# Kernel tuning notes

Measured on AMD Instinct MI355X. Metric: run time of the kernel, lower is better.

Reference implementation:

```python
import jax, jax.numpy as jnp
import numpy as np

D, D_SEQ, D_HEAD, N_HEAD = 256, 1280, 48, 8
N_NODE, B_GRAPH, S_LEN = 2048, 8, 1024
HDH = N_HEAD * D_HEAD  # 384
SCALE = float(np.sqrt(D_HEAD))
LN_EPS = 1e-5


def setup_inputs() -> dict:
    key = jax.random.key(0)
    ks = jax.random.split(key, 12)
    node = jax.random.normal(ks[0], (N_NODE, D), dtype=jnp.float32)
    emb = jax.random.normal(ks[1], (B_GRAPH, S_LEN, D_SEQ), dtype=jnp.float32)
    mask = jax.random.randint(ks[2], (B_GRAPH, S_LEN), 0, 2, dtype=jnp.int32)
    batch = jnp.sort(jax.random.randint(ks[3], (N_NODE,), 0, B_GRAPH, dtype=jnp.int64))
    def lin(k, fan_in, fan_out):
        lim = 1.0 / np.sqrt(fan_in)
        return jax.random.uniform(k, (fan_in, fan_out), jnp.float32, -lim, lim)
    return {
        "node": node,
        "packed_sequence_emb": emb,
        "packed_sequence_mask": mask,
        "batch": batch,
        "ln_g": jnp.ones((D,), jnp.float32),
        "ln_b": jnp.zeros((D,), jnp.float32),
        "Wq": lin(ks[4], D, HDH),
        "Wk": lin(ks[5], D_SEQ, HDH),
        "Wv": lin(ks[6], D_SEQ, HDH),
        "Wg": lin(ks[7], D, HDH),
        "bg": jnp.zeros((HDH,), jnp.float32),
        "Wback": lin(ks[8], HDH, D),
        "bback": jnp.zeros((D,), jnp.float32),
    }


def _layernorm(x, g, b):
    mu = jnp.mean(x, axis=-1, keepdims=True)
    var = jnp.mean(jnp.square(x - mu), axis=-1, keepdims=True)
    return (x - mu) * jax.lax.rsqrt(var + LN_EPS) * g + b


def reference(node, packed_sequence_emb, packed_sequence_mask, batch,
              ln_g, ln_b, Wq, Wk, Wv, Wg, bg, Wback, bback):
    N = node.shape[0]
    y = _layernorm(node, ln_g, ln_b)                                   # [N, D]
    q = (y @ Wq).reshape(N, N_HEAD, D_HEAD)                            # [N, H, Dh]
    k = (packed_sequence_emb @ Wk).reshape(B_GRAPH, S_LEN, N_HEAD, D_HEAD)
    v = (packed_sequence_emb @ Wv).reshape(B_GRAPH, S_LEN, N_HEAD, D_HEAD)

    # scores[n, s, h] = <q[n,h], k[batch[n], s, h]> / sqrt(Dh)
    scores_all = jnp.einsum('nhd,bshd->nbsh', q, k) / SCALE            # [N, B, S, H]
    scores = jnp.take_along_axis(
        scores_all, batch[:, None, None, None].astype(jnp.int32), axis=1
    )[:, 0]                                                            # [N, S, H]

    # masked softmax over sequence axis (dim=1), mask broadcast over heads
    mask_f = packed_sequence_mask[batch].astype(scores.dtype)[:, :, None]  # [N, S, 1]
    s_max = jnp.max(jnp.where(mask_f > 0, scores, -jnp.inf), axis=1, keepdims=True)
    e = jnp.exp(scores - s_max) * mask_f
    w = e / (jnp.sum(e, axis=1, keepdims=True) + 1e-9)                 # [N, S, H]

    # out[n,h,d] = sum_s w[n,s,h] * v[batch[n], s, h, d]
    feat_all = jnp.einsum('nsh,bshd->nbhd', w, v)                      # [N, B, H, Dh]
    feat = jnp.take_along_axis(
        feat_all, batch[:, None, None, None].astype(jnp.int32), axis=1
    )[:, 0]                                                            # [N, H, Dh]

    gate = jax.nn.sigmoid(y @ Wg + bg).reshape(N, N_HEAD, D_HEAD)
    new = (gate * feat).reshape(N, HDH) @ Wback + bback
    return node + new
```

## Files before the change

### kernel.cpp

```cpp
#include <hip/hip_runtime.h>
#include <hip/hip_bf16.h>
#include <math.h>

#define D 256
#define D_SEQ 1280
#define D_HEAD 48
#define N_HEAD 8
#define HDH 384
#define N_NODE 2048
#define B_GRAPH 8
#define S_LEN 1024
#define LN_EPS 1e-5f
#define QSCALE (0.14433756729740643f * 1.4426950408889634f)
#define KVN 768
#define QGN 768
#define QROWS (N_NODE + 16)
#define TPG 40
#define NWL (TPG * 8)
#define PAD_T 164864

typedef unsigned short u16;
typedef __attribute__((ext_vector_type(8))) short short8;
typedef __attribute__((ext_vector_type(4))) short short4v;
typedef __attribute__((ext_vector_type(4))) unsigned short ushort4v;
typedef __attribute__((ext_vector_type(4))) float floatx4;

__device__ __forceinline__ u16 f2bf(float f) {
    unsigned int x = __float_as_uint(f);
    x += 0x7fff + ((x >> 16) & 1);
    return (u16)(x >> 16);
}

__device__ __forceinline__ void load_lds16(const u16* g, u16* lds) {
    __builtin_amdgcn_global_load_lds(
        (const __attribute__((address_space(1))) unsigned int*)g,
        (__attribute__((address_space(3))) unsigned int*)lds, 16, 0, 0);
}

__global__ __launch_bounds__(256)
void prep(const float* __restrict__ emb, u16* __restrict__ embb,
          const float* __restrict__ node, const float* __restrict__ ln_g,
          const float* __restrict__ ln_b, u16* __restrict__ yb,
          const float* __restrict__ Wk, const float* __restrict__ Wv,
          const float* __restrict__ Wq, const float* __restrict__ Wg,
          const float* __restrict__ Wback,
          u16* __restrict__ WT, u16* __restrict__ WT2, u16* __restrict__ WbT,
          const int* __restrict__ batch, const int* __restrict__ mask,
          int* __restrict__ ranges, int* __restrict__ wl,
          int* __restrict__ kvwl, int* __restrict__ scnt,
          u16* __restrict__ Kp, u16* __restrict__ Qb) {
    const int bx = blockIdx.x;
    const int tid = threadIdx.x;
    if (bx < 512) {
        const int b = bx >> 6, chunk = bx & 63;
        __shared__ unsigned long long words[16];
        __shared__ int wpre[17];
        #pragma unroll
        for (int c = 0; c < 4; ++c) {
            const int s = c * 256 + tid;
            const unsigned long long bal = __ballot(mask[b * S_LEN + s] != 0);
            if ((tid & 63) == 0) words[c * 4 + (tid >> 6)] = bal;
        }
        __syncthreads();
        if (tid == 0) {
            int a = 0;
            #pragma unroll
            for (int w = 0; w < 16; ++w) { wpre[w] = a; a += __popcll(words[w]); }
            wpre[16] = a;
        }
        __syncthreads();
        const int cnt = wpre[16];
        const int ce = (cnt + 127) & ~127;
        const int r = chunk * 16 + (tid >> 4);
        const int sub = tid & 15;
        const unsigned long long w = words[r >> 6];
        const bool on = (w >> (r & 63)) & 1ull;
        if (on) {
            const int rank = wpre[r >> 6] +
                __popcll(w & ((1ull << (r & 63)) - 1ull));
            const float* src = &emb[((size_t)b * S_LEN + r) * D_SEQ];
            u16* dst = &embb[((size_t)b * S_LEN + rank) * D_SEQ];
            #pragma unroll
            for (int it = 0; it < 10; ++it) {
                const int off = it * 128 + sub * 8;
                const float4 a = *(const float4*)&src[off];
                const float4 b4 = *(const float4*)&src[off + 4];
                union { u16 u[8]; int4 v; } p;
                p.u[0]=f2bf(a.x); p.u[1]=f2bf(a.y); p.u[2]=f2bf(a.z); p.u[3]=f2bf(a.w);
                p.u[4]=f2bf(b4.x); p.u[5]=f2bf(b4.y); p.u[6]=f2bf(b4.z); p.u[7]=f2bf(b4.w);
                *(int4*)&dst[off] = p.v;
            }
        }
        const int c2 = chunk * 16 + (tid >> 4);
        if (c2 >= cnt && c2 < ce) {
            u16* dst = &embb[((size_t)b * S_LEN + c2) * D_SEQ];
            const int4 z = {0, 0, 0, 0};
            #pragma unroll
            for (int it = 0; it < 10; ++it)
                *(int4*)&dst[it * 128 + sub * 8] = z;
        }
        return;
    }
    if (bx < 2560) {
        const int n = bx - 512, t = tid;
        float x = node[n * D + t];
        float s = x, sq = x * x;
        #pragma unroll
        for (int o = 32; o > 0; o >>= 1) {
            s  += __shfl_down(s, o);
            sq += __shfl_down(sq, o);
        }
        __shared__ float ss[4], sqs[4];
        if ((t & 63) == 0) { ss[t >> 6] = s; sqs[t >> 6] = sq; }
        __syncthreads();
        float S  = ss[0] + ss[1] + ss[2] + ss[3];
        float SQ = sqs[0] + sqs[1] + sqs[2] + sqs[3];
        float mu  = S * (1.f / D);
        float var = SQ * (1.f / D) - mu * mu;
        float inv = rsqrtf(var + LN_EPS);
        yb[n * D + t] = f2bf((x - mu) * inv * ln_g[t] + ln_b[t]);
        return;
    }
    if (bx < 3808) {
        int u = bx - 2560;
        const float* W; u16* WTo; int K, kx, ny, Ncols;
        if (u < 480)      { W = Wk;    WTo = WT;                       K = D_SEQ; Ncols = HDH; kx = u % 40; ny = u / 40; }
        else if (u < 960) { u -= 480;  W = Wv; WTo = WT + (size_t)HDH * D_SEQ; K = D_SEQ; Ncols = HDH; kx = u % 40; ny = u / 40; }
        else if (u < 1056){ u -= 960;  W = Wq; WTo = WT2;              K = D;   Ncols = HDH; kx = u % 8;  ny = u / 8; }
        else if (u < 1152){ u -= 1056; W = Wg; WTo = WT2 + (size_t)HDH * D; K = D; Ncols = HDH; kx = u % 8; ny = u / 8; }
        else              { u -= 1152; W = Wback; WTo = WbT;           K = HDH; Ncols = D;   kx = u % 12; ny = u / 12; }
        const int k0 = kx * 32, n0 = ny * 32;
        __shared__ float tile[32][33];
        const int tx = tid & 31, ty = tid >> 5;
        #pragma unroll
        for (int i = 0; i < 32; i += 8)
            tile[ty + i][tx] = W[(size_t)(k0 + ty + i) * Ncols + n0 + tx];
        __syncthreads();
        #pragma unroll
        for (int i = 0; i < 32; i += 8)
            WTo[(size_t)(n0 + ty + i) * K + k0 + tx] = f2bf(tile[tx][ty + i]);
        return;
    }
    if (bx == 3808) {
        const int t = tid;
        __shared__ int msum[8][32];
        __shared__ int mcnt[8];
        const int g = t >> 5, ii = t & 31;
        int p = 0;
        #pragma unroll
        for (int k = 0; k < 32; ++k) p += mask[g * S_LEN + k * 32 + ii];
        msum[g][ii] = p;
        if (t <= B_GRAPH) {
            int lo = 0, hi = N_NODE;
            while (lo < hi) {
                int mid = (lo + hi) >> 1;
                if (batch[mid] < t) lo = mid + 1; else hi = mid;
            }
            ranges[t] = lo;
        }
        __syncthreads();
        if (t < 8) {
            int s = 0;
            #pragma unroll
            for (int k = 0; k < 32; ++k) s += msum[t][k];
            mcnt[t] = s;
            scnt[t] = s;
        }
        __syncthreads();
        if (t < B_GRAPH) {
            const int s = ranges[t];
            const int ntile = (ranges[t + 1] - s + 15) >> 4;
            for (int i = 0; i < TPG; ++i)
                wl[i * 8 + t] = (i < ntile) ? ((t << 16) | (s + i * 16)) : -1;
            const int tc = (mcnt[t] + 127) >> 7;
            for (int i = 0; i < 8; ++i)
                kvwl[i * 8 + t] = (i < tc) ? (t * S_LEN + i * 128) : -1;
        }
        return;
    }
    const int t = (bx - 3809) * 256 + tid;
    const int4 z = {0, 0, 0, 0};
    if (t < 131072) {
        const int row = t >> 1, half = t & 1;
        *(int4*)&Kp[(size_t)row * 64 + 48 + half * 8] = z;
    } else if (t < 164096) {
        const int u = t - 131072;
        const int row = u >> 1, half = u & 1;
        *(int4*)&Qb[(size_t)row * 64 + 48 + half * 8] = z;
    } else {
        const int u = t - 164096;
        const int row = u / 6, c = u - row * 6;
        const int hh = row >> 4, m = 2048 + (row & 15);
        *(int4*)&Qb[((size_t)hh * QROWS + m) * 64 + c * 8] = z;
    }
}

__global__ __launch_bounds__(256)
void kvqg_gemm(const u16* __restrict__ A, const u16* __restrict__ WT,
               u16* __restrict__ Kp, u16* __restrict__ V4,
               const u16* __restrict__ Ab, const u16* __restrict__ WT2,
               const float* __restrict__ bg, u16* __restrict__ Qb,
               float* __restrict__ gate, const int* __restrict__ kvwl) {
    __shared__ __align__(16) u16 As[128 * 32];
    __shared__ __align__(16) u16 Bs[64 * 32];
    const int tid = threadIdx.x;
    const int lane = tid & 63, wave = tid >> 6;
    const int wm64 = (wave >> 1) * 64, wn32 = (wave & 1) * 32;
    const int lm = lane & 15, lq = lane >> 4;

    if (blockIdx.x < 768) {
        const int e = kvwl[blockIdx.x / 12];
        if (e < 0) return;
        const int m0 = e;
        const int n0 = (blockIdx.x % 12) * 64;

        floatx4 acc[4][2] = {};

        const int srow = lane >> 2, scol = (lane & 3) * 8;
        const u16* ag  = &A[(size_t)(m0 + wave * 16 + srow) * D_SEQ + scol];
        const u16* ag2 = ag + (size_t)64 * D_SEQ;
        const u16* bgp = &WT[(size_t)(n0 + wave * 16 + srow) * D_SEQ + scol];
        u16* asb  = &As[wave * 512];
        u16* asb2 = &As[2048 + wave * 512];
        u16* bsb  = &Bs[wave * 512];

        for (int k0 = 0; k0 < D_SEQ; k0 += 32) {
            __syncthreads();
            load_lds16(ag + k0, asb);
            load_lds16(ag2 + k0, asb2);
            load_lds16(bgp + k0, bsb);
            __syncthreads();

            short8 af[4], bfr[2];
            #pragma unroll
            for (int i = 0; i < 4; ++i)
                af[i] = *(const short8*)&As[(wm64 + i * 16 + lm) * 32 + lq * 8];
            #pragma unroll
            for (int j = 0; j < 2; ++j)
                bfr[j] = *(const short8*)&Bs[(wn32 + j * 16 + lm) * 32 + lq * 8];
            #pragma unroll
            for (int i = 0; i < 4; ++i)
                #pragma unroll
                for (int j = 0; j < 2; ++j)
                    acc[i][j] = __builtin_amdgcn_mfma_f32_16x16x32_bf16(
                        af[i], bfr[j], acc[i][j], 0, 0, 0);
        }

        #pragma unroll
        for (int i = 0; i < 4; ++i) {
            const int mrow = m0 + wm64 + i * 16 + lq * 4;
            const int bb = mrow >> 10, s = mrow & 1023;
            #pragma unroll
            for (int j = 0; j < 2; ++j) {
                const int n = n0 + wn32 + j * 16 + lm;
                if (n < HDH) {
                    const int hh = n / 48, dd = n - hh * 48;
                    u16* kp = &Kp[(((size_t)(bb * N_HEAD + hh)) * S_LEN + s) * 64 + dd];
                    kp[0]   = f2bf(acc[i][j][0]);
                    kp[64]  = f2bf(acc[i][j][1]);
                    kp[128] = f2bf(acc[i][j][2]);
                    kp[192] = f2bf(acc[i][j][3]);
                } else {
                    const int nv = n - HDH;
                    const int hh = nv / 48, dd = nv - hh * 48;
                    ushort4v pk;
                    pk[0] = f2bf(acc[i][j][0]); pk[1] = f2bf(acc[i][j][1]);
                    pk[2] = f2bf(acc[i][j][2]); pk[3] = f2bf(acc[i][j][3]);
                    *(ushort4v*)&V4[(((size_t)(bb * N_HEAD + hh)) * (S_LEN / 4) + (s >> 2)) * 192 + dd * 4] = pk;
                }
            }
        }
        return;
    }

    {
        const int u = blockIdx.x - 768;
        const int m0 = (u / 12) * 128, n0 = (u % 12) * 64;

        floatx4 acc[4][2] = {};
        const int sr = tid >> 2;
        const int sc = (tid & 3) * 8;

        for (int k0 = 0; k0 < D; k0 += 32) {
            const int4 a0 = *(const int4*)&Ab[(size_t)(m0 + sr) * D + k0 + sc];
            const int4 a1 = *(const int4*)&Ab[(size_t)(m0 + sr + 64) * D + k0 + sc];
            const int4 b0 = *(const int4*)&WT2[(size_t)(n0 + sr) * D + k0 + sc];
            __syncthreads();
            *(int4*)&As[sr * 32 + sc] = a0;
            *(int4*)&As[(sr + 64) * 32 + sc] = a1;
            *(int4*)&Bs[sr * 32 + sc] = b0;
            __syncthreads();

            short8 af[4], bfr[2];
            #pragma unroll
            for (int i = 0; i < 4; ++i)
                af[i] = *(const short8*)&As[(wm64 + i * 16 + lm) * 32 + lq * 8];
            #pragma unroll
            for (int j = 0; j < 2; ++j)
                bfr[j] = *(const short8*)&Bs[(wn32 + j * 16 + lm) * 32 + lq * 8];
            #pragma unroll
            for (int i = 0; i < 4; ++i)
                #pragma unroll
                for (int j = 0; j < 2; ++j)
                    acc[i][j] = __builtin_amdgcn_mfma_f32_16x16x32_bf16(
                        af[i], bfr[j], acc[i][j], 0, 0, 0);
        }

        #pragma unroll
        for (int i = 0; i < 4; ++i) {
            const int mb = m0 + wm64 + i * 16 + lq * 4;
            #pragma unroll
            for (int j = 0; j < 2; ++j) {
                const int n = n0 + wn32 + j * 16 + lm;
                #pragma unroll
                for (int r = 0; r < 4; ++r) {
                    const int m = mb + r;
                    const float v = acc[i][j][r];
                    if (n < HDH) {
                        const int hh = n / 48, dd = n - hh * 48;
                        Qb[((size_t)hh * QROWS + m) * 64 + dd] = f2bf(v * QSCALE);
                    } else {
                        const int ng = n - HDH;
                        gate[(size_t)m * HDH + ng] = 1.f / (1.f + __expf(-(v + bg[ng])));
                    }
                }
            }
        }
    }
}

__global__ __launch_bounds__(256)
void back_gemm(const u16* __restrict__ Ab, const u16* __restrict__ Bt,
               const float* __restrict__ bias, const float* __restrict__ resid,
               float* __restrict__ C) {
    __shared__ __align__(16) u16 As[128 * 32];
    __shared__ __align__(16) u16 Bs[64 * 32];
    const int tid = threadIdx.x;
    const int lane = tid & 63, wave = tid >> 6;
    const int wm = (wave >> 1) * 64, wn = (wave & 1) * 32;
    const int m0 = blockIdx.y * 128, n0 = blockIdx.x * 64;
    const int lm = lane & 15, lq = lane >> 4;

    floatx4 acc[4][2] = {};
    const int sr = tid >> 2;
    const int sc = (tid & 3) * 8;

    for (int k0 = 0; k0 < HDH; k0 += 32) {
        const int4 a0 = *(const int4*)&Ab[(size_t)(m0 + sr) * HDH + k0 + sc];
        const int4 a1 = *(const int4*)&Ab[(size_t)(m0 + sr + 64) * HDH + k0 + sc];
        const int4 b0 = *(const int4*)&Bt[(size_t)(n0 + sr) * HDH + k0 + sc];
        __syncthreads();
        *(int4*)&As[sr * 32 + sc] = a0;
        *(int4*)&As[(sr + 64) * 32 + sc] = a1;
        *(int4*)&Bs[sr * 32 + sc] = b0;
        __syncthreads();

        short8 af[4], bfr[2];
        #pragma unroll
        for (int i = 0; i < 4; ++i)
            af[i] = *(const short8*)&As[(wm + i * 16 + lm) * 32 + lq * 8];
        #pragma unroll
        for (int j = 0; j < 2; ++j)
            bfr[j] = *(const short8*)&Bs[(wn + j * 16 + lm) * 32 + lq * 8];
        #pragma unroll
        for (int i = 0; i < 4; ++i)
            #pragma unroll
            for (int j = 0; j < 2; ++j)
                acc[i][j] = __builtin_amdgcn_mfma_f32_16x16x32_bf16(
                    af[i], bfr[j], acc[i][j], 0, 0, 0);
    }

    #pragma unroll
    for (int i = 0; i < 4; ++i) {
        const int mb = m0 + wm + i * 16 + lq * 4;
        #pragma unroll
        for (int j = 0; j < 2; ++j) {
            const int n = n0 + wn + j * 16 + lm;
            #pragma unroll
            for (int r = 0; r < 4; ++r) {
                const int m = mb + r;
                C[(size_t)m * D + n] = acc[i][j][r] + bias[n] + resid[(size_t)m * D + n];
            }
        }
    }
}

struct Pref {
    short8 k0, k1;
    short4v v0, v1, v2;
};

__device__ __forceinline__ Pref ldpref(const u16* kbase, const u16* vbase,
                                       int s, int lm, int lq) {
    Pref p;
    const u16* kr = &kbase[(size_t)(s + lm) * 64];
    p.k0 = *(const short8*)&kr[lq * 8];
    p.k1 = *(const short8*)&kr[32 + lq * 8];
    const size_t vo = (size_t)((s >> 2) + lq) * 192;
    p.v0 = *(const short4v*)&vbase[vo];
    p.v1 = *(const short4v*)&vbase[vo + 64];
    p.v2 = *(const short4v*)&vbase[vo + 128];
    return p;
}

__global__ __launch_bounds__(256)
void attn_mfma(const u16* __restrict__ Qb, const u16* __restrict__ Kp,
               const u16* __restrict__ V4, const int* __restrict__ scnt,
               const int* __restrict__ ranges, const int* __restrict__ wl,
               const float* __restrict__ gate, u16* __restrict__ gfeatb) {
    const int e = wl[blockIdx.x];
    if (e < 0) return;
    const int b = e >> 16, n0 = e & 0xffff;
    const int h = blockIdx.y;
    const int nend = ranges[b + 1];
    const int NT = min(16, nend - n0);

    const int tid = threadIdx.x;
    const int wave = tid >> 6, lane = tid & 63;
    const int lm = lane & 15, lq = lane >> 4;
    const int bh = b * N_HEAD + h;

    const u16* qrow = &Qb[((size_t)h * QROWS + n0 + lm) * 64];
    const short8 qf0 = *(const short8*)&qrow[lq * 8];
    const short8 qf1 = *(const short8*)&qrow[32 + lq * 8];

    const u16* kbase = &Kp[(size_t)bh * S_LEN * 64];
    const u16* vbase = &V4[(size_t)bh * (S_LEN / 4) * 192 + (size_t)lm * 4];

    const int cnt = scnt[b];
    const int T = (cnt + 15) >> 4;
    const int j = wave;
    const int nt = (j < T) ? (((T - 1 - j) >> 2) + 1) : 0;

    float l_i = 0.f;
    floatx4 acc0 = {}, acc1 = {}, acc2 = {};

    Pref pA, pB;
    if (nt > 0) pA = ldpref(kbase, vbase, j * 16, lm, lq);
    if (nt > 1) pB = ldpref(kbase, vbase, (j + 4) * 16, lm, lq);

    int t = 0;
    auto step = [&](Pref& P) {
        const int s0 = (j + t * 4) * 16;
        floatx4 st = {};
        st = __builtin_amdgcn_mfma_f32_16x16x32_bf16(P.k0, qf0, st, 0, 0, 0);
        st = __builtin_amdgcn_mfma_f32_16x16x32_bf16(P.k1, qf1, st, 0, 0, 0);
        const short4v v0 = P.v0, v1 = P.v1, v2 = P.v2;
        if (t + 2 < nt) P = ldpref(kbase, vbase, (j + (t + 2) * 4) * 16, lm, lq);

        const int rem = cnt - s0 - lq * 4;
        const float p0 = rem > 0 ? exp2f(st[0]) : 0.f;
        const float p1 = rem > 1 ? exp2f(st[1]) : 0.f;
        const float p2 = rem > 2 ? exp2f(st[2]) : 0.f;
        const float p3 = rem > 3 ? exp2f(st[3]) : 0.f;
        l_i += (p0 + p1) + (p2 + p3);

        union { __hip_bfloat162 h2[2]; short4v v; } pu;
        pu.h2[0] = __float22bfloat162_rn(make_float2(p0, p1));
        pu.h2[1] = __float22bfloat162_rn(make_float2(p2, p3));

        acc0 = __builtin_amdgcn_mfma_f32_16x16x16bf16_1k(v0, pu.v, acc0, 0, 0, 0);
        acc1 = __builtin_amdgcn_mfma_f32_16x16x16bf16_1k(v1, pu.v, acc1, 0, 0, 0);
        acc2 = __builtin_amdgcn_mfma_f32_16x16x16bf16_1k(v2, pu.v, acc2, 0, 0, 0);
        ++t;
    };
    while (t < nt) {
        step(pA);
        if (t < nt) step(pB);
    }

    l_i += __shfl_xor(l_i, 16);
    l_i += __shfl_xor(l_i, 32);

    __shared__ float sl[4][64];
    __shared__ float sacc[4][3][4][64];
    sl[wave][lane] = l_i;
    #pragma unroll
    for (int r = 0; r < 4; ++r) {
        sacc[wave][0][r][lane] = acc0[r];
        sacc[wave][1][r][lane] = acc1[r];
        sacc[wave][2][r][lane] = acc2[r];
    }
    __syncthreads();
    if (wave < 3 && lm < NT) {
        const int dt = wave;
        const float L = sl[0][lane] + sl[1][lane] + sl[2][lane] + sl[3][lane];
        const float inv = 1.f / (L + 1e-9f);
        const size_t o = (size_t)(n0 + lm) * HDH + h * 48 + dt * 16 + lq * 4;
        const float4 g = *(const float4*)&gate[o];
        float4 ov;
        ov.x = sacc[0][dt][0][lane] + sacc[1][dt][0][lane] +
               sacc[2][dt][0][lane] + sacc[3][dt][0][lane];
        ov.y = sacc[0][dt][1][lane] + sacc[1][dt][1][lane] +
               sacc[2][dt][1][lane] + sacc[3][dt][1][lane];
        ov.z = sacc[0][dt][2][lane] + sacc[1][dt][2][lane] +
               sacc[2][dt][2][lane] + sacc[3][dt][2][lane];
        ov.w = sacc[0][dt][3][lane] + sacc[1][dt][3][lane] +
               sacc[2][dt][3][lane] + sacc[3][dt][3][lane];
        union { __hip_bfloat162 h2[2]; ushort4v v; } r2;
        r2.h2[0] = __float22bfloat162_rn(make_float2(ov.x * inv * g.x,
                                                     ov.y * inv * g.y));
        r2.h2[1] = __float22bfloat162_rn(make_float2(ov.z * inv * g.z,
                                                     ov.w * inv * g.w));
        *(ushort4v*)&gfeatb[o] = r2.v;
    }
}

extern "C" void kernel_launch(void* const* d_in, const int* in_sizes, int n_in,
                              void* d_out, int out_size, void* d_ws, size_t ws_size,
                              hipStream_t stream) {
    const float* node  = (const float*)d_in[0];
    const float* emb   = (const float*)d_in[1];
    const int*   mask  = (const int*)d_in[2];
    const int*   batch = (const int*)d_in[3];
    const float* ln_g  = (const float*)d_in[4];
    const float* ln_b  = (const float*)d_in[5];
    const float* Wq    = (const float*)d_in[6];
    const float* Wk    = (const float*)d_in[7];
    const float* Wv    = (const float*)d_in[8];
    const float* Wg    = (const float*)d_in[9];
    const float* bg    = (const float*)d_in[10];
    const float* Wback = (const float*)d_in[11];
    const float* bback = (const float*)d_in[12];
    float* out = (float*)d_out;

    float* ws    = (float*)d_ws;
    float* gate  = ws;
    float* Pacc  = gate + (size_t)N_NODE * HDH;
    float* Pl    = Pacc + (size_t)2 * N_NODE * HDH;
    u16*   gfeatb = (u16*)(Pl + (size_t)2 * N_NODE * N_HEAD);
    u16*   yb    = gfeatb + (size_t)N_NODE * HDH;
    u16*   WT    = yb + (size_t)N_NODE * D;
    u16*   WT2   = WT + (size_t)KVN * D_SEQ;
    u16*   WbT   = WT2 + (size_t)QGN * D;
    u16*   Qb    = WbT + (size_t)D * HDH;
    u16*   Kp    = Qb + (size_t)N_HEAD * QROWS * 64;
    u16*   V4    = Kp + (size_t)B_GRAPH * N_HEAD * S_LEN * 64;
    u16*   embb  = V4 + (size_t)B_GRAPH * N_HEAD * (S_LEN / 4) * 192;
    int*   ranges = (int*)(embb + (size_t)B_GRAPH * S_LEN * D_SEQ);
    int*   wl    = ranges + 16;
    int*   kvwl  = wl + NWL;
    int*   scnt  = kvwl + 64;

    prep<<<3809 + PAD_T / 256, 256, 0, stream>>>(
        emb, embb, node, ln_g, ln_b, yb, Wk, Wv, Wq, Wg, Wback,
        WT, WT2, WbT, batch, mask, ranges, wl, kvwl, scnt, Kp, Qb);
    kvqg_gemm<<<960, 256, 0, stream>>>(embb, WT, Kp, V4, yb, WT2, bg, Qb, gate, kvwl);
    attn_mfma<<<dim3(NWL, N_HEAD), 256, 0, stream>>>(
        Qb, Kp, V4, scnt, ranges, wl, gate, gfeatb);
    back_gemm<<<dim3(D / 64, N_NODE / 128), 256, 0, stream>>>(
        gfeatb, WbT, bback, node, out);
}
```

Before: 167.7 us.

## Load GEMM fragments directly from global into registers with double-buffered prefetch

All three GEMM kernels (KV, QG, back-projection) stop staging A/B tiles through LDS and instead load MFMA fragments straight from global memory into registers. Two k-steps are prefetched ahead. This removes the __syncthreads barriers and LDS round trips. The cost is that waves sharing the same rows no longer share loaded tiles, so global/L2 traffic goes up, and each lane's loads are 16-byte pieces from strided rows, which coalesce less well. Register pressure also rises from holding two fragment sets.

```diff
diff --git a/kernel.cpp b/kernel.cpp
--- a/kernel.cpp
+++ b/kernel.cpp
@@ -29,12 +29,6 @@
     unsigned int x = __float_as_uint(f);
     x += 0x7fff + ((x >> 16) & 1);
     return (u16)(x >> 16);
-}
-
-__device__ __forceinline__ void load_lds16(const u16* g, u16* lds) {
-    __builtin_amdgcn_global_load_lds(
-        (const __attribute__((address_space(1))) unsigned int*)g,
-        (__attribute__((address_space(3))) unsigned int*)lds, 16, 0, 0);
 }
 
 __global__ __launch_bounds__(256)
@@ -195,14 +189,42 @@
     }
 }
 
+struct GFrag {
+    short8 a0, a1, a2, a3;
+    short8 b0, b1;
+};
+
+__device__ __forceinline__ GFrag gld(const u16* pa0, const u16* pa1,
+                                     const u16* pa2, const u16* pa3,
+                                     const u16* pb0, const u16* pb1, int k) {
+    GFrag f;
+    f.a0 = *(const short8*)(pa0 + k);
+    f.a1 = *(const short8*)(pa1 + k);
+    f.a2 = *(const short8*)(pa2 + k);
+    f.a3 = *(const short8*)(pa3 + k);
+    f.b0 = *(const short8*)(pb0 + k);
+    f.b1 = *(const short8*)(pb1 + k);
+    return f;
+}
+
+#define GSTEP(F)                                                              \
+    do {                                                                      \
+        acc[0][0] = __builtin_amdgcn_mfma_f32_16x16x32_bf16((F).a0, (F).b0, acc[0][0], 0, 0, 0); \
+        acc[0][1] = __builtin_amdgcn_mfma_f32_16x16x32_bf16((F).a0, (F).b1, acc[0][1], 0, 0, 0); \
+        acc[1][0] = __builtin_amdgcn_mfma_f32_16x16x32_bf16((F).a1, (F).b0, acc[1][0], 0, 0, 0); \
+        acc[1][1] = __builtin_amdgcn_mfma_f32_16x16x32_bf16((F).a1, (F).b1, acc[1][1], 0, 0, 0); \
+        acc[2][0] = __builtin_amdgcn_mfma_f32_16x16x32_bf16((F).a2, (F).b0, acc[2][0], 0, 0, 0); \
+        acc[2][1] = __builtin_amdgcn_mfma_f32_16x16x32_bf16((F).a2, (F).b1, acc[2][1], 0, 0, 0); \
+        acc[3][0] = __builtin_amdgcn_mfma_f32_16x16x32_bf16((F).a3, (F).b0, acc[3][0], 0, 0, 0); \
+        acc[3][1] = __builtin_amdgcn_mfma_f32_16x16x32_bf16((F).a3, (F).b1, acc[3][1], 0, 0, 0); \
+    } while (0)
+
 __global__ __launch_bounds__(256)
 void kvqg_gemm(const u16* __restrict__ A, const u16* __restrict__ WT,
                u16* __restrict__ Kp, u16* __restrict__ V4,
                const u16* __restrict__ Ab, const u16* __restrict__ WT2,
                const float* __restrict__ bg, u16* __restrict__ Qb,
                float* __restrict__ gate, const int* __restrict__ kvwl) {
-    __shared__ __align__(16) u16 As[128 * 32];
-    __shared__ __align__(16) u16 Bs[64 * 32];
     const int tid = threadIdx.x;
     const int lane = tid & 63, wave = tid >> 6;
     const int wm64 = (wave >> 1) * 64, wn32 = (wave & 1) * 32;
@@ -216,34 +238,22 @@
 
         floatx4 acc[4][2] = {};
 
-        const int srow = lane >> 2, scol = (lane & 3) * 8;
-        const u16* ag  = &A[(size_t)(m0 + wave * 16 + srow) * D_SEQ + scol];
-        const u16* ag2 = ag + (size_t)64 * D_SEQ;
-        const u16* bgp = &WT[(size_t)(n0 + wave * 16 + srow) * D_SEQ + scol];
-        u16* asb  = &As[wave * 512];
-        u16* asb2 = &As[2048 + wave * 512];
-        u16* bsb  = &Bs[wave * 512];
-
-        for (int k0 = 0; k0 < D_SEQ; k0 += 32) {
-            __syncthreads();
-            load_lds16(ag + k0, asb);
-            load_lds16(ag2 + k0, asb2);
-            load_lds16(bgp + k0, bsb);
-            __syncthreads();
-
-            short8 af[4], bfr[2];
-            #pragma unroll
-            for (int i = 0; i < 4; ++i)
-                af[i] = *(const short8*)&As[(wm64 + i * 16 + lm) * 32 + lq * 8];
-            #pragma unroll
-            for (int j = 0; j < 2; ++j)
-                bfr[j] = *(const short8*)&Bs[(wn32 + j * 16 + lm) * 32 + lq * 8];
-            #pragma unroll
-            for (int i = 0; i < 4; ++i)
-                #pragma unroll
-                for (int j = 0; j < 2; ++j)
-                    acc[i][j] = __builtin_amdgcn_mfma_f32_16x16x32_bf16(
-                        af[i], bfr[j], acc[i][j], 0, 0, 0);
+        const u16* pa0 = &A[(size_t)(m0 + wm64 + lm) * D_SEQ + lq * 8];
+        const u16* pa1 = pa0 + (size_t)16 * D_SEQ;
+        const u16* pa2 = pa0 + (size_t)32 * D_SEQ;
+        const u16* pa3 = pa0 + (size_t)48 * D_SEQ;
+        const u16* pb0 = &WT[(size_t)(n0 + wn32 + lm) * D_SEQ + lq * 8];
+        const u16* pb1 = pb0 + (size_t)16 * D_SEQ;
+
+        GFrag pA = gld(pa0, pa1, pa2, pa3, pb0, pb1, 0);
+        GFrag pB = gld(pa0, pa1, pa2, pa3, pb0, pb1, 32);
+        for (int k = 0; k < D_SEQ; k += 64) {
+            GFrag cur = pA;
+            if (k + 64 < D_SEQ) pA = gld(pa0, pa1, pa2, pa3, pb0, pb1, k + 64);
+            GSTEP(cur);
+            GFrag cur2 = pB;
+            if (k + 96 < D_SEQ) pB = gld(pa0, pa1, pa2, pa3, pb0, pb1, k + 96);
+            GSTEP(cur2);
         }
 
         #pragma unroll
@@ -278,32 +288,23 @@
         const int m0 = (u / 12) * 128, n0 = (u % 12) * 64;
 
         floatx4 acc[4][2] = {};
-        const int sr = tid >> 2;
-        const int sc = (tid & 3) * 8;
-
-        for (int k0 = 0; k0 < D; k0 += 32) {
-            const int4 a0 = *(const int4*)&Ab[(size_t)(m0 + sr) * D + k0 + sc];
-            const int4 a1 = *(const int4*)&Ab[(size_t)(m0 + sr + 64) * D + k0 + sc];
-            const int4 b0 = *(const int4*)&WT2[(size_t)(n0 + sr) * D + k0 + sc];
-            __syncthreads();
-            *(int4*)&As[sr * 32 + sc] = a0;
-            *(int4*)&As[(sr + 64) * 32 + sc] = a1;
-            *(int4*)&Bs[sr * 32 + sc] = b0;
-            __syncthreads();
-
-            short8 af[4], bfr[2];
-            #pragma unroll
-            for (int i = 0; i < 4; ++i)
-                af[i] = *(const short8*)&As[(wm64 + i * 16 + lm) * 32 + lq * 8];
-            #pragma unroll
-            for (int j = 0; j < 2; ++j)
-                bfr[j] = *(const short8*)&Bs[(wn32 + j * 16 + lm) * 32 + lq * 8];
-            #pragma unroll
-            for (int i = 0; i < 4; ++i)
-                #pragma unroll
-                for (int j = 0; j < 2; ++j)
-                    acc[i][j] = __builtin_amdgcn_mfma_f32_16x16x32_bf16(
-                        af[i], bfr[j], acc[i][j], 0, 0, 0);
+
+        const u16* pa0 = &Ab[(size_t)(m0 + wm64 + lm) * D + lq * 8];
+        const u16* pa1 = pa0 + (size_t)16 * D;
+        const u16* pa2 = pa0 + (size_t)32 * D;
+        const u16* pa3 = pa0 + (size_t)48 * D;
+        const u16* pb0 = &WT2[(size_t)(n0 + wn32 + lm) * D + lq * 8];
+        const u16* pb1 = pb0 + (size_t)16 * D;
+
+        GFrag pA = gld(pa0, pa1, pa2, pa3, pb0, pb1, 0);
+        GFrag pB = gld(pa0, pa1, pa2, pa3, pb0, pb1, 32);
+        for (int k = 0; k < D; k += 64) {
+            GFrag cur = pA;
+            if (k + 64 < D) pA = gld(pa0, pa1, pa2, pa3, pb0, pb1, k + 64);
+            GSTEP(cur);
+            GFrag cur2 = pB;
+            if (k + 96 < D) pB = gld(pa0, pa1, pa2, pa3, pb0, pb1, k + 96);
+            GSTEP(cur2);
         }
 
         #pragma unroll
@@ -333,49 +334,38 @@
 void back_gemm(const u16* __restrict__ Ab, const u16* __restrict__ Bt,
                const float* __restrict__ bias, const float* __restrict__ resid,
                float* __restrict__ C) {
-    __shared__ __align__(16) u16 As[128 * 32];
-    __shared__ __align__(16) u16 Bs[64 * 32];
     const int tid = threadIdx.x;
     const int lane = tid & 63, wave = tid >> 6;
-    const int wm = (wave >> 1) * 64, wn = (wave & 1) * 32;
+    const int wm64 = (wave >> 1) * 64, wn32 = (wave & 1) * 32;
     const int m0 = blockIdx.y * 128, n0 = blockIdx.x * 64;
     const int lm = lane & 15, lq = lane >> 4;
 
     floatx4 acc[4][2] = {};
-    const int sr = tid >> 2;
-    const int sc = (tid & 3) * 8;
-
-    for (int k0 = 0; k0 < HDH; k0 += 32) {
-        const int4 a0 = *(const int4*)&Ab[(size_t)(m0 + sr) * HDH + k0 + sc];
-        const int4 a1 = *(const int4*)&Ab[(size_t)(m0 + sr + 64) * HDH + k0 + sc];
-        const int4 b0 = *(const int4*)&Bt[(size_t)(n0 + sr) * HDH + k0 + sc];
-        __syncthreads();
-        *(int4*)&As[sr * 32 + sc] = a0;
-        *(int4*)&As[(sr + 64) * 32 + sc] = a1;
-        *(int4*)&Bs[sr * 32 + sc] = b0;
-        __syncthreads();
-
-        short8 af[4], bfr[2];
-        #pragma unroll
-        for (int i = 0; i < 4; ++i)
-            af[i] = *(const short8*)&As[(wm + i * 16 + lm) * 32 + lq * 8];
-        #pragma unroll
-        for (int j = 0; j < 2; ++j)
-            bfr[j] = *(const short8*)&Bs[(wn + j * 16 + lm) * 32 + lq * 8];
-        #pragma unroll
-        for (int i = 0; i < 4; ++i)
-            #pragma unroll
-            for (int j = 0; j < 2; ++j)
-                acc[i][j] = __builtin_amdgcn_mfma_f32_16x16x32_bf16(
-                    af[i], bfr[j], acc[i][j], 0, 0, 0);
+
+    const u16* pa0 = &Ab[(size_t)(m0 + wm64 + lm) * HDH + lq * 8];
+    const u16* pa1 = pa0 + (size_t)16 * HDH;
+    const u16* pa2 = pa0 + (size_t)32 * HDH;
+    const u16* pa3 = pa0 + (size_t)48 * HDH;
+    const u16* pb0 = &Bt[(size_t)(n0 + wn32 + lm) * HDH + lq * 8];
+    const u16* pb1 = pb0 + (size_t)16 * HDH;
+
+    GFrag pA = gld(pa0, pa1, pa2, pa3, pb0, pb1, 0);
+    GFrag pB = gld(pa0, pa1, pa2, pa3, pb0, pb1, 32);
+    for (int k = 0; k < HDH; k += 64) {
+        GFrag cur = pA;
+        if (k + 64 < HDH) pA = gld(pa0, pa1, pa2, pa3, pb0, pb1, k + 64);
+        GSTEP(cur);
+        GFrag cur2 = pB;
+        if (k + 96 < HDH) pB = gld(pa0, pa1, pa2, pa3, pb0, pb1, k + 96);
+        GSTEP(cur2);
     }
 
     #pragma unroll
     for (int i = 0; i < 4; ++i) {
-        const int mb = m0 + wm + i * 16 + lq * 4;
+        const int mb = m0 + wm64 + i * 16 + lq * 4;
         #pragma unroll
         for (int j = 0; j < 2; ++j) {
-            const int n = n0 + wn + j * 16 + lm;
+            const int n = n0 + wn32 + j * 16 + lm;
             #pragma unroll
             for (int r = 0; r < 4; ++r) {
                 const int m = mb + r;
```

Measured after the change: 200.3 us. +19.4%, slower.
